# Optimization experiments

Measured on AMD Instinct MI355X. Metric: run time of the kernel, lower is better.

The kernel has to match this reference:

```python
import jax, jax.numpy as jnp
import numpy as np
from functools import partial

HIDDEN = 1024
NT = 4096


def setup_inputs() -> dict:
    key = jax.random.key(0)
    k1, k2, k3, k4 = jax.random.split(key, 4)
    # PyTorch nn.Linear default init ~ U(-1/sqrt(fan_in), 1/sqrt(fan_in)); use small
    # normal weights for numerical stability over 4096 recurrent steps.
    W1 = jax.random.normal(k1, (1, HIDDEN), dtype=jnp.float32) * 0.05
    b1 = jax.random.normal(k2, (HIDDEN,), dtype=jnp.float32) * 0.05
    W2 = jax.random.normal(k3, (HIDDEN, 1), dtype=jnp.float32) * 0.05
    b2 = jax.random.normal(k4, (1,), dtype=jnp.float32) * 0.05
    x0 = jnp.ones((1,), dtype=jnp.float32)            # x_m[0:1] in source
    dt = jnp.full((1,), 2.0 / (NT - 1), dtype=jnp.float32)  # linspace(0,2,nt) spacing
    return {"x0": x0, "dt": dt, "nt": NT, "W1": W1, "b1": b1, "W2": W2, "b2": b2}


def reference(x0, dt, nt, W1, b1, W2, b2):
    dt_s = dt[0]

    def nn(x):  # x: [1] -> [1]; Linear(1,H) -> ReLU -> Linear(H,1)
        h = jnp.maximum(x @ W1 + b1, 0.0)  # [H]
        return h @ W2 + b2                  # [1]

    def step(x_k, _):
        x_next = x_k + dt_s * nn(x_k)
        return x_next, x_next

    _, outs = jax.lax.scan(step, x0, None, length=nt - 1)  # outs: [nt-1, 1]
    x_pred = jnp.concatenate([x0, outs[:, 0]])             # [nt]
    return x_pred
```

## Files before the change

### kernel.cpp

```cpp
#include <hip/hip_runtime.h>
#include <math.h>

#define UPL 16
#define NTH 512
#define MAXRUNS 512

#define DPPMV(v, ctrl) __int_as_float(__builtin_amdgcn_update_dpp( \
    __float_as_int(v), __float_as_int(v), (ctrl), 0xf, 0xf, false))

__device__ inline float wave_min64(float v) {
    v = fminf(v, DPPMV(v, 0x111));
    v = fminf(v, DPPMV(v, 0x112));
    v = fminf(v, DPPMV(v, 0x114));
    v = fminf(v, DPPMV(v, 0x118));
    v = fminf(v, DPPMV(v, 0x142));
    v = fminf(v, DPPMV(v, 0x143));
    return __int_as_float(__builtin_amdgcn_readlane(__float_as_int(v), 63));
}
__device__ inline float wave_max64(float v) {
    v = fmaxf(v, DPPMV(v, 0x111));
    v = fmaxf(v, DPPMV(v, 0x112));
    v = fmaxf(v, DPPMV(v, 0x114));
    v = fmaxf(v, DPPMV(v, 0x118));
    v = fmaxf(v, DPPMV(v, 0x142));
    v = fmaxf(v, DPPMV(v, 0x143));
    return __int_as_float(__builtin_amdgcn_readlane(__float_as_int(v), 63));
}

__device__ inline double geo_val(double xs, double delta, double L2, double m) {
    double t = m * L2;
    if (fabs(t) < 0.043) {
        double e = t * 0.6931471805599453094;
        double g = e * (1.0 + e * (0.5 + e * (1.0/6.0 + e * (1.0/24.0 + e * (1.0/120.0 + e * (1.0/720.0))))));
        return (xs + delta) + delta * g;
    }
    return xs + delta * (double)exp2f((float)t);
}
__device__ inline double lin_val(double xst, double d, double m) { return fma(m, d, xst); }

__global__ __launch_bounds__(NTH) void euler_kernel(
    const float* __restrict__ x0p, const float* __restrict__ dtp,
    const float* __restrict__ W1, const float* __restrict__ b1,
    const float* __restrict__ W2, const float* __restrict__ b2p,
    float* __restrict__ out, int nt)
{
    __shared__ int    s_k0[MAXRUNS];
    __shared__ double s_p0[MAXRUNS], s_p1[MAXRUNS], s_p2[MAXRUNS];
    __shared__ unsigned char s_ln[MAXRUNS];
    __shared__ int s_nr, s_fe;

    const int tid = threadIdx.x;
    const float x0f = x0p[0];
    const float INFF = __builtin_huge_valf();

    if (tid < 64) {
        const int lane = tid;
        const float dtf = dtp[0], b2 = b2p[0];

        float tk[UPL], da[UPL], dc[UPL];
        double accA = 0.0, accB = 0.0;
        #pragma unroll
        for (int i = 0; i < UPL; ++i) {
            int u = i * 64 + lane;
            float w1 = W1[u], bb = b1[u], w2 = W2[u];
            float a = w1 * w2, cc = bb * w2;
            float key, d_a, d_c;
            if (w1 > 0.0f)      { key = -bb / w1; d_a =  a; d_c =  cc; }
            else if (w1 < 0.0f) { key = -bb / w1; d_a = -a; d_c = -cc; accA += (double)a; accB += (double)cc; }
            else                { key = INFF;     d_a = 0.0f; d_c = 0.0f; accB += (double)(fmaxf(bb, 0.0f) * w2); }
            tk[i] = key; da[i] = d_a; dc[i] = d_c;
            if (key <= x0f) { accA += (double)d_a; accB += (double)d_c; }
        }
        #pragma unroll
        for (int off = 32; off; off >>= 1) {
            accA += __shfl_xor(accA, off);
            accB += __shfl_xor(accB, off);
        }
        double A = accA, B = accB + (double)b2;

        const double dt = (double)dtf;
        double x = (double)x0f;
        float  xf = x0f;
        int k = 0, r = 0, fend = 0;
        const int last = nt - 1;

        while (k < last && r < MAXRUNS) {
            double eps = dt * A, d = dt * B;
            double v = eps * x + d;
            int remaining = last - k;
            int m, lin; double P0, P1, P2;

            if (v == 0.0) { lin = 1; P0 = x; P1 = 0.0; P2 = 0.0; m = remaining; }
            else {
                const bool up = (v > 0.0);
                float T;
                if (up) {
                    float q0 = INFF, q1 = INFF, q2 = INFF, q3 = INFF;
                    #pragma unroll
                    for (int i = 0; i < UPL; i += 4) {
                        q0 = fminf(q0, (tk[i    ] > xf) ? tk[i    ] : INFF);
                        q1 = fminf(q1, (tk[i + 1] > xf) ? tk[i + 1] : INFF);
                        q2 = fminf(q2, (tk[i + 2] > xf) ? tk[i + 2] : INFF);
                        q3 = fminf(q3, (tk[i + 3] > xf) ? tk[i + 3] : INFF);
                    }
                    T = wave_min64(fminf(fminf(q0, q1), fminf(q2, q3)));
                } else {
                    float q0 = -INFF, q1 = -INFF, q2 = -INFF, q3 = -INFF;
                    #pragma unroll
                    for (int i = 0; i < UPL; i += 4) {
                        q0 = fmaxf(q0, (tk[i    ] < xf) ? tk[i    ] : -INFF);
                        q1 = fmaxf(q1, (tk[i + 1] < xf) ? tk[i + 1] : -INFF);
                        q2 = fmaxf(q2, (tk[i + 2] < xf) ? tk[i + 2] : -INFF);
                        q3 = fmaxf(q3, (tk[i + 3] < xf) ? tk[i + 3] : -INFF);
                    }
                    T = wave_max64(fmaxf(fmaxf(q0, q1), fmaxf(q2, q3)));
                }
                const double Td = (double)T;

                if (eps == 0.0) {
                    lin = 1; P0 = x; P1 = d; P2 = 0.0;
                    if (isinf(T)) m = remaining;
                    else {
                        double mm = (Td - x) / d;
                        m = (mm < (double)remaining) ? ((mm < 1.0) ? 1 : (int)ceil(mm)) : remaining;
                        int g = 0;
                        while (m < remaining && g++ < 8) { double y = lin_val(P0, P1, (double)m);     if (up ? (y >= Td) : (y <= Td)) break; ++m; }
                        g = 0;
                        while (m > 1 && g++ < 8)         { double y = lin_val(P0, P1, (double)(m-1)); if (up ? (y >= Td) : (y <= Td)) --m; else break; }
                    }
                } else {
                    lin = 0;
                    double r0 = (double)__builtin_amdgcn_rcpf((float)eps);
                    r0 = r0 * (2.0 - eps * r0);
                    r0 = r0 * (2.0 - eps * r0);
                    double xs = -d * r0;
                    double delta = x - xs;
                    double L2 = eps * (1.0 - eps * (0.5 - eps * (1.0/3.0 - eps * 0.25)))
                              * 1.4426950408889634074;
                    P0 = xs; P1 = delta; P2 = L2;
                    if (isinf(T)) m = remaining;
                    else {
                        float uf  = (float)(Td - x) * __builtin_amdgcn_rcpf((float)delta);
                        float mmf = __log2f(1.0f + uf) / (float)L2;
                        if (!(mmf < (float)remaining)) m = remaining;
                        else m = (mmf < 1.0f) ? 1 : (int)ceilf(mmf);
                        double ym = geo_val(P0, P1, P2, (double)m);
                        int g = 0;
                        while (m < remaining && g++ < 8) {
                            if (up ? (ym >= Td) : (ym <= Td)) break;
                            ++m; ym = geo_val(P0, P1, P2, (double)m);
                        }
                        g = 0;
                        while (m > 1 && g++ < 8) {
                            double yp = geo_val(P0, P1, P2, (double)(m - 1));
                            if (up ? (yp >= Td) : (yp <= Td)) --m; else break;
                        }
                    }
                }
            }

            if (lane == 0) {
                s_k0[r] = k; s_ln[r] = (unsigned char)lin;
                s_p0[r] = P0; s_p1[r] = P1; s_p2[r] = P2;
            }
            ++r;
            double xn = lin ? lin_val(P0, P1, (double)m) : geo_val(P0, P1, P2, (double)m);
            k += m; fend = k;
            float xnf = (float)xn;

            if (k < last) {
                float sA = 0.0f, sB = 0.0f; int cnt = 0;
                bool upm = (xnf > xf);
                #pragma unroll
                for (int i = 0; i < UPL; ++i) {
                    float tv = tk[i];
                    bool in = upm ? (tv > xf && tv <= xnf) : (tv > xnf && tv <= xf);
                    if (in) { sA += da[i]; sB += dc[i]; ++cnt; }
                }
                unsigned long long msk = __ballot(cnt > 0);
                double dsA = 0.0, dsB = 0.0;
                while (msk) {
                    int l = __ffsll(msk) - 1;
                    msk &= (msk - 1);
                    dsA += (double)__shfl(sA, l);
                    dsB += (double)__shfl(sB, l);
                }
                if (upm) { A += dsA; B += dsB; } else { A -= dsA; B -= dsB; }
            }
            x = xn; xf = xnf;
        }

        while (k < last) {
            double eps = dt * A, d = dt * B;
            double xn = x + (eps * x + d);
            ++k;
            if (lane == 0) out[k] = (float)xn;
            float xnf = (float)xn;
            float sA = 0.0f, sB = 0.0f;
            bool upm = (xnf > xf);
            #pragma unroll
            for (int i = 0; i < UPL; ++i) {
                float tv = tk[i];
                bool in = upm ? (tv > xf && tv <= xnf) : (tv > xnf && tv <= xf);
                if (in) { sA += da[i]; sB += dc[i]; }
            }
            #pragma unroll
            for (int off = 32; off; off >>= 1) {
                sA += __shfl_xor(sA, off);
                sB += __shfl_xor(sB, off);
            }
            if (upm) { A += (double)sA; B += (double)sB; }
            else     { A -= (double)sA; B -= (double)sB; }
            x = xn; xf = xnf;
        }

        if (lane == 0) { s_nr = r; s_fe = fend; }
    }
    __syncthreads();

    {
        const int nr = s_nr, fe = s_fe;
        for (int kk = tid; kk <= fe; kk += NTH) {
            if (kk == 0) { out[0] = x0f; continue; }
            int lo = 0, hi = nr - 1;
            while (lo < hi) {
                int mid = (lo + hi + 1) >> 1;
                if (s_k0[mid] < kk) lo = mid; else hi = mid - 1;
            }
            double m = (double)(kk - s_k0[lo]);
            double vv = s_ln[lo] ? lin_val(s_p0[lo], s_p1[lo], m)
                                 : geo_val(s_p0[lo], s_p1[lo], s_p2[lo], m);
            out[kk] = (float)vv;
        }
    }
}

extern "C" void kernel_launch(void* const* d_in, const int* in_sizes, int n_in,
                              void* d_out, int out_size, void* d_ws, size_t ws_size,
                              hipStream_t stream) {
    const float* x0 = (const float*)d_in[0];
    const float* dt = (const float*)d_in[1];
    const float* W1 = (const float*)d_in[3];
    const float* b1 = (const float*)d_in[4];
    const float* W2 = (const float*)d_in[5];
    const float* b2 = (const float*)d_in[6];
    float* out = (float*)d_out;
    const int nt = out_size;
    euler_kernel<<<1, NTH, 0, stream>>>(x0, dt, W1, b1, W2, b2, out, nt);
}
```

Measured before the change: 25.42 us.

## Vectorize weight loads, DPP double reductions, and wave-parallel crossing search

Loads W1, b1 and W2 as float4 and replaces the shuffle-based double reductions with DPP-based wave sums. The serial geometric-run crossing search, which stepped m up and down one at a time, becomes a wave-parallel scan: each of the 64 lanes evaluates one candidate step and a ballot finds the first crossing. This cuts the serial latency per run in the single-wave recurrence loop. The new search falls back to m=remaining after 8 windows, which could change results in edge cases. The float4 loads also change which lane owns which hidden unit, so consistency with the unseen later per-unit code is uncertain.

```diff
diff --git a/kernel.cpp b/kernel.cpp
--- a/kernel.cpp
+++ b/kernel.cpp
@@ -25,6 +25,26 @@
     v = fmaxf(v, DPPMV(v, 0x142));
     v = fmaxf(v, DPPMV(v, 0x143));
     return __int_as_float(__builtin_amdgcn_readlane(__float_as_int(v), 63));
+}
+
+template<int CTRL>
+__device__ inline double ddpp0(double v) {
+    long long l = __double_as_longlong(v);
+    int lo = __builtin_amdgcn_update_dpp(0, (int)(l & 0xffffffffLL), CTRL, 0xf, 0xf, true);
+    int hi = __builtin_amdgcn_update_dpp(0, (int)(l >> 32),          CTRL, 0xf, 0xf, true);
+    return __longlong_as_double(((long long)hi << 32) | (unsigned long long)(unsigned)lo);
+}
+__device__ inline double wave_dsum64(double v) {
+    v += ddpp0<0x111>(v);
+    v += ddpp0<0x112>(v);
+    v += ddpp0<0x114>(v);
+    v += ddpp0<0x118>(v);
+    v += ddpp0<0x142>(v);
+    v += ddpp0<0x143>(v);
+    long long l = __double_as_longlong(v);
+    int lo = __builtin_amdgcn_readlane((int)(l & 0xffffffffLL), 63);
+    int hi = __builtin_amdgcn_readlane((int)(l >> 32), 63);
+    return __longlong_as_double(((long long)hi << 32) | (unsigned long long)(unsigned)lo);
 }
 
 __device__ inline double geo_val(double xs, double delta, double L2, double m) {
@@ -59,24 +79,32 @@
 
         float tk[UPL], da[UPL], dc[UPL];
         double accA = 0.0, accB = 0.0;
+        const float4* W14 = (const float4*)W1;
+        const float4* B14 = (const float4*)b1;
+        const float4* W24 = (const float4*)W2;
         #pragma unroll
-        for (int i = 0; i < UPL; ++i) {
-            int u = i * 64 + lane;
-            float w1 = W1[u], bb = b1[u], w2 = W2[u];
-            float a = w1 * w2, cc = bb * w2;
-            float key, d_a, d_c;
-            if (w1 > 0.0f)      { key = -bb / w1; d_a =  a; d_c =  cc; }
-            else if (w1 < 0.0f) { key = -bb / w1; d_a = -a; d_c = -cc; accA += (double)a; accB += (double)cc; }
-            else                { key = INFF;     d_a = 0.0f; d_c = 0.0f; accB += (double)(fmaxf(bb, 0.0f) * w2); }
-            tk[i] = key; da[i] = d_a; dc[i] = d_c;
-            if (key <= x0f) { accA += (double)d_a; accB += (double)d_c; }
-        }
-        #pragma unroll
-        for (int off = 32; off; off >>= 1) {
-            accA += __shfl_xor(accA, off);
-            accB += __shfl_xor(accB, off);
-        }
-        double A = accA, B = accB + (double)b2;
+        for (int i = 0; i < UPL / 4; ++i) {
+            float4 w1v = W14[i * 64 + lane];
+            float4 b1v = B14[i * 64 + lane];
+            float4 w2v = W24[i * 64 + lane];
+            float w1a[4] = {w1v.x, w1v.y, w1v.z, w1v.w};
+            float b1a[4] = {b1v.x, b1v.y, b1v.z, b1v.w};
+            float w2a[4] = {w2v.x, w2v.y, w2v.z, w2v.w};
+            #pragma unroll
+            for (int j = 0; j < 4; ++j) {
+                int idx = i * 4 + j;
+                float w1 = w1a[j], bb = b1a[j], w2 = w2a[j];
+                float a = w1 * w2, cc = bb * w2;
+                float key, d_a, d_c;
+                if (w1 > 0.0f)      { key = -bb / w1; d_a =  a; d_c =  cc; }
+                else if (w1 < 0.0f) { key = -bb / w1; d_a = -a; d_c = -cc; accA += (double)a; accB += (double)cc; }
+                else                { key = INFF;     d_a = 0.0f; d_c = 0.0f; accB += (double)(fmaxf(bb, 0.0f) * w2); }
+                tk[idx] = key; da[idx] = d_a; dc[idx] = d_c;
+                if (key <= x0f) { accA += (double)d_a; accB += (double)d_c; }
+            }
+        }
+        double A = wave_dsum64(accA);
+        double B = wave_dsum64(accB) + (double)b2;
 
         const double dt = (double)dtf;
         double x = (double)x0f;
@@ -142,18 +170,33 @@
                     else {
                         float uf  = (float)(Td - x) * __builtin_amdgcn_rcpf((float)delta);
                         float mmf = __log2f(1.0f + uf) / (float)L2;
-                        if (!(mmf < (float)remaining)) m = remaining;
-                        else m = (mmf < 1.0f) ? 1 : (int)ceilf(mmf);
-                        double ym = geo_val(P0, P1, P2, (double)m);
-                        int g = 0;
-                        while (m < remaining && g++ < 8) {
-                            if (up ? (ym >= Td) : (ym <= Td)) break;
-                            ++m; ym = geo_val(P0, P1, P2, (double)m);
-                        }
-                        g = 0;
-                        while (m > 1 && g++ < 8) {
-                            double yp = geo_val(P0, P1, P2, (double)(m - 1));
-                            if (up ? (yp >= Td) : (yp <= Td)) --m; else break;
+                        if (!(mmf < (float)remaining + 8.0f)) m = remaining;
+                        else {
+                            float msf = mmf - 8.0f;
+                            int mstart = (msf > 1.0f) ? (int)msf : 1;
+                            m = 0;
+                            bool firstTry = true;
+                            #pragma unroll 1
+                            for (int t = 0; t < 8 && m == 0; ++t) {
+                                if (mstart >= remaining) { m = remaining; break; }
+                                double y = geo_val(P0, P1, P2, (double)(mstart + lane));
+                                bool crossed = up ? (y >= Td) : (y <= Td);
+                                unsigned long long cm = __ballot(crossed);
+                                if (cm) {
+                                    int idx = __ffsll(cm) - 1;
+                                    if (idx == 0 && mstart > 1 && firstTry) {
+                                        mstart = (mstart > 64) ? (mstart - 64) : 1;
+                                        firstTry = false;
+                                        continue;
+                                    }
+                                    int mcf = mstart + idx;
+                                    m = (mcf < remaining) ? mcf : remaining;
+                                } else {
+                                    mstart += 64;
+                                    firstTry = false;
+                                }
+                            }
+                            if (m == 0) m = remaining;
                         }
                     }
                 }
```

After: 29.68 us. +16.8%, slower.
